# Kernel tuning notes

Hardware: AMD Instinct MI355X
Metric: run time of the kernel (lower is better)

Reference implementation:

```python
import jax, jax.numpy as jnp
import numpy as np

D_MODEL = 2048
NUM_HEADS = 16
HEAD_DIM = D_MODEL // NUM_HEADS
LAYER_IDX = 0
NUM_LAYERS = 13
REINIT_LAMBDA = 0.8


def setup_inputs() -> dict:
    key = jax.random.key(0)
    ks = jax.random.split(key, 8)
    B, S = 2, 2048
    x = jax.random.normal(ks[0], (B, S, D_MODEL), dtype=jnp.float32)
    init = 1.0 / np.sqrt(D_MODEL)
    def w(k):
        return jax.random.uniform(k, (D_MODEL, D_MODEL), dtype=jnp.float32, minval=-init, maxval=init)
    lam_init = REINIT_LAMBDA * ((LAYER_IDX + 1) / NUM_LAYERS)
    return {
        "x": x,
        "q1_w": w(ks[1]), "k1_w": w(ks[2]),
        "q2_w": w(ks[3]), "k2_w": w(ks[4]),
        "v_w": w(ks[5]), "o_w": w(ks[6]),
        "lambda_param": jnp.full((NUM_HEADS,), lam_init, dtype=jnp.float32),
    }


def _heads(t, B, S):
    # [B, S, D] -> [B, H, S, Dh]
    return t.reshape(B, S, NUM_HEADS, HEAD_DIM).transpose(0, 2, 1, 3)


def reference(x, q1_w, k1_w, q2_w, k2_w, v_w, o_w, lambda_param):
    B, S, _ = x.shape
    # nn.Linear(bias=False): y = x @ W.T, W is [out, in]
    q1 = _heads(x @ q1_w.T, B, S)
    k1 = _heads(x @ k1_w.T, B, S)
    q2 = _heads(x @ q2_w.T, B, S)
    k2 = _heads(x @ k2_w.T, B, S)
    v = _heads(x @ v_w.T, B, S)
    scale = jnp.sqrt(jnp.float32(HEAD_DIM))
    attn1 = jax.nn.softmax(jnp.einsum('bhqd,bhkd->bhqk', q1, k1) / scale, axis=-1)
    attn2 = jax.nn.softmax(jnp.einsum('bhqd,bhkd->bhqk', q2, k2) / scale, axis=-1)
    lam = lambda_param.reshape(1, NUM_HEADS, 1, 1)
    out = jnp.einsum('bhqk,bhkd->bhqd', attn1 - lam * attn2, v)
    out = out.transpose(0, 2, 1, 3).reshape(B, S, D_MODEL)
    return out @ o_w.T
```

## Files before the change

### kernel.cpp

```cpp
#include <hip/hip_runtime.h>
#include <hip/hip_bf16.h>
#include <stdint.h>

typedef __bf16 bf16_t;
typedef __bf16 bf16x8 __attribute__((ext_vector_type(8)));
typedef float f32x4 __attribute__((ext_vector_type(4)));

#define D_MODEL 2048
#define SEQ     2048
#define NHEADS  16
#define HDIM    128
#define BATCH   2
#define NTOK    (BATCH * SEQ)
#define NELEM   ((size_t)BATCH * SEQ * D_MODEL)
#define D2      ((size_t)D_MODEL * D_MODEL)

__global__ void __launch_bounds__(256)
cvt7_kernel(const float* __restrict__ x,
            const float* __restrict__ w0, const float* __restrict__ w1,
            const float* __restrict__ w2, const float* __restrict__ w3,
            const float* __restrict__ w4, const float* __restrict__ w5,
            bf16_t* __restrict__ xb, bf16_t* __restrict__ wb) {
  const int y = blockIdx.y;
  const float* srcs[7] = {x, w0, w1, w2, w3, w4, w5};
  const float* src = srcs[y];
  bf16_t* dst = (y == 0) ? xb : wb + (size_t)(y - 1) * D2;
  const size_t n = (y == 0) ? NELEM : D2;
  const size_t base = ((size_t)blockIdx.x * 256 + threadIdx.x) * 8;
  if (base >= n) return;
  f32x4 lo = *(const f32x4*)(src + base);
  f32x4 hi = *(const f32x4*)(src + base + 4);
  union { bf16x8 v; bf16_t h[8]; } u;
#pragma unroll
  for (int j = 0; j < 4; j++) {
    u.h[j]     = (bf16_t)lo[j];
    u.h[j + 4] = (bf16_t)hi[j];
  }
  *(bf16x8*)(dst + base) = u.v;
}

__device__ __forceinline__ void async_load16(const void* g, void* l) {
  __builtin_amdgcn_global_load_lds(
      (const __attribute__((address_space(1))) void*)g,
      (__attribute__((address_space(3))) void*)l, 16, 0, 0);
}

template <int TRANS, typename TC>
__device__ __forceinline__ void gemm_tile_body(const bf16_t* __restrict__ A,
                                               const bf16_t* __restrict__ W,
                                               TC* __restrict__ C) {
  extern __shared__ char smem[];
  bf16_t* As = (bf16_t*)smem;
  bf16_t* Bs = (bf16_t*)smem + 128 * 32;
  const int K = D_MODEL, N = D_MODEL;
  const int tid  = threadIdx.x;
  const int wave = tid >> 6, lane = tid & 63;
  const int quad = lane >> 4, l16 = lane & 15;
  const int tm = blockIdx.x * 128, tn = blockIdx.y * 128;
  const int wm = (wave & 1) * 64, wn = (wave >> 1) * 64;

  f32x4 acc[4][4];
#pragma unroll
  for (int i = 0; i < 4; i++)
#pragma unroll
    for (int j = 0; j < 4; j++) acc[i][j] = (f32x4){0.f, 0.f, 0.f, 0.f};

  const int srow = lane >> 2;
  const int scol = (lane & 3) * 8;

  for (int k0 = 0; k0 < K; k0 += 32) {
    __syncthreads();
#pragma unroll
    for (int i = 0; i < 2; i++) {
      const int rbase = (i * 4 + wave) * 16;
      async_load16(A + (size_t)(tm + rbase + srow) * K + k0 + scol, As + rbase * 32);
      async_load16(W + (size_t)(tn + rbase + srow) * K + k0 + scol, Bs + rbase * 32);
    }
    __syncthreads();

    bf16x8 af[4], bfr[4];
#pragma unroll
    for (int i = 0; i < 4; i++)
      af[i] = *(const bf16x8*)(As + (wm + i * 16 + l16) * 32 + quad * 8);
#pragma unroll
    for (int j = 0; j < 4; j++)
      bfr[j] = *(const bf16x8*)(Bs + (wn + j * 16 + l16) * 32 + quad * 8);
#pragma unroll
    for (int i = 0; i < 4; i++)
#pragma unroll
      for (int j = 0; j < 4; j++)
        acc[i][j] = __builtin_amdgcn_mfma_f32_16x16x32_bf16(af[i], bfr[j], acc[i][j], 0, 0, 0);
  }

#pragma unroll
  for (int i = 0; i < 4; i++) {
    const int r0 = wm + i * 16 + quad * 4;
#pragma unroll
    for (int j = 0; j < 4; j++) {
      const int c = tn + wn + j * 16 + l16;
      if constexpr (TRANS) {
        const int m = tm + r0;
        const int b = m >> 11;
        const int s = m & (SEQ - 1);
        union { bf16_t h[4]; uint2 u2; } p;
#pragma unroll
        for (int r = 0; r < 4; r++) p.h[r] = (bf16_t)acc[i][j][r];
        *(uint2*)((bf16_t*)C + (size_t)(b * D_MODEL + c) * SEQ + s) = p.u2;
      } else {
#pragma unroll
        for (int r = 0; r < 4; r++)
          C[(size_t)(tm + r0 + r) * N + c] = (TC)acc[i][j][r];
      }
    }
  }
}

__global__ void __launch_bounds__(256)
gemm_out_kernel(const bf16_t* __restrict__ A, const bf16_t* __restrict__ W,
                float* __restrict__ C) {
  gemm_tile_body<0, float>(A, W, C);
}

template <int TRANS, typename TC>
__device__ __forceinline__ void gemm256_body(const bf16_t* __restrict__ A,
                                             const bf16_t* __restrict__ W,
                                             TC* __restrict__ C,
                                             const int tm, const int tn) {
  extern __shared__ char smem[];
  constexpr int K = D_MODEL;
  constexpr int NT = K / 64;
  const int tid = threadIdx.x;
  const int wid = tid >> 6, lane = tid & 63;
  const int quad = lane >> 4, l16 = lane & 15;
  const int wm = wid >> 2, wn = wid & 3;

  const int sr = lane >> 2;
  const int sc = (lane & 3) ^ ((lane >> 4) & 2);
  const int rdoff = (l16 * 64 + quad * 16) ^ ((l16 & 8) << 2);

  f32x4 acc[8][4];
#pragma unroll
  for (int i = 0; i < 8; i++)
#pragma unroll
    for (int j = 0; j < 4; j++) acc[i][j] = (f32x4){0.f, 0.f, 0.f, 0.f};

  bf16x8 af[2][4], bfA[2][2], bfB[2][2];

#define STAGE256(P, rowbase, ldsbase, h, t)                                      \
  {                                                                              \
    const bf16_t* _s = (P) + (size_t)((rowbase) + (h) * 128 + wid * 16 + sr) * K \
                           + ((t) * 64 + sc * 8);                                \
    char* _d = smem + (ldsbase) + (h) * 16384 + wid * 2048;                      \
    async_load16(_s, _d);                                                        \
    async_load16(_s + 32, _d + 1024);                                            \
  }

#define LDA256(c, rh)                                                            \
  _Pragma("unroll") for (int ks = 0; ks < 2; ks++)                               \
  _Pragma("unroll") for (int j = 0; j < 4; j++)                                  \
      af[ks][j] = *(const bf16x8*)(smem + (c) * 65536 +                          \
                  ((wm * 8 + (rh) * 4 + j) * 2 + ks) * 1024 + rdoff);

#define LDB256(c, dst, cf0)                                                      \
  _Pragma("unroll") for (int ks = 0; ks < 2; ks++)                               \
  _Pragma("unroll") for (int j = 0; j < 2; j++)                                  \
      dst[ks][j] = *(const bf16x8*)(smem + (c) * 65536 + 32768 +                 \
                   ((wn * 4 + (cf0) + j) * 2 + ks) * 1024 + rdoff);

#define MFMA16(rh, bfr, cb)                                                      \
  _Pragma("unroll") for (int j = 0; j < 4; j++)                                  \
  _Pragma("unroll") for (int cf = 0; cf < 2; cf++)                               \
  _Pragma("unroll") for (int ks = 0; ks < 2; ks++)                               \
      acc[(rh) * 4 + j][(cb) + cf] = __builtin_amdgcn_mfma_f32_16x16x32_bf16(    \
          af[ks][j], bfr[ks][cf], acc[(rh) * 4 + j][(cb) + cf], 0, 0, 0);

#define BAR256() __builtin_amdgcn_s_barrier()
#define LGKM0()                                                                  \
  { asm volatile("s_waitcnt lgkmcnt(0)" ::: "memory");                           \
    __builtin_amdgcn_sched_barrier(0); }
#define VMW4()                                                                   \
  { asm volatile("s_waitcnt vmcnt(4)" ::: "memory");                             \
    __builtin_amdgcn_sched_barrier(0); }
#define VMW0()                                                                   \
  { asm volatile("s_waitcnt vmcnt(0)" ::: "memory");                             \
    __builtin_amdgcn_sched_barrier(0); }

  STAGE256(A, tm, 0,     0, 0); STAGE256(A, tm, 0,     1, 0);
  STAGE256(W, tn, 32768, 0, 0); STAGE256(W, tn, 32768, 1, 0);
  STAGE256(W, tn, 98304, 0, 1); STAGE256(W, tn, 98304, 1, 1);
  VMW4();
  BAR256();

  for (int it = 0; it < NT / 2; ++it) {
    const int kt = 2 * it;
    const int t2 = (kt + 2 < NT) ? kt + 2 : 0;
    const int t3 = (kt + 3 < NT) ? kt + 3 : 0;

    LDA256(0, 0); LDB256(0, bfA, 0);
    STAGE256(A, tm, 65536, 0, kt + 1);
    BAR256(); LGKM0();
    __builtin_amdgcn_s_setprio(1); MFMA16(0, bfA, 0); __builtin_amdgcn_s_setprio(0);
    BAR256();
    LDB256(0, bfB, 2);
    STAGE256(A, tm, 65536, 1, kt + 1);
    BAR256(); LGKM0();
    __builtin_amdgcn_s_setprio(1); MFMA16(0, bfB, 2); __builtin_amdgcn_s_setprio(0);
    BAR256();
    LDA256(0, 1);
    STAGE256(W, tn, 32768, 0, t2);
    BAR256(); LGKM0();
    __builtin_amdgcn_s_setprio(1); MFMA16(1, bfA, 0); __builtin_amdgcn_s_setprio(0);
    BAR256();
    STAGE256(W, tn, 32768, 1, t2);
    BAR256();
    __builtin_amdgcn_s_setprio(1); MFMA16(1, bfB, 2); __builtin_amdgcn_s_setprio(0);
    VMW4();
    BAR256();
    LDA256(1, 0); LDB256(1, bfA, 0);
    STAGE256(A, tm, 0, 0, t2);
    BAR256(); LGKM0();
    __builtin_amdgcn_s_setprio(1); MFMA16(0, bfA, 0); __builtin_amdgcn_s_setprio(0);
    BAR256();
    LDB256(1, bfB, 2);
    STAGE256(A, tm, 0, 1, t2);
    BAR256(); LGKM0();
    __builtin_amdgcn_s_setprio(1); MFMA16(0, bfB, 2); __builtin_amdgcn_s_setprio(0);
    BAR256();
    LDA256(1, 1);
    STAGE256(W, tn, 98304, 0, t3);
    BAR256(); LGKM0();
    __builtin_amdgcn_s_setprio(1); MFMA16(1, bfA, 0); __builtin_amdgcn_s_setprio(0);
    BAR256();
    STAGE256(W, tn, 98304, 1, t3);
    BAR256();
    __builtin_amdgcn_s_setprio(1); MFMA16(1, bfB, 2); __builtin_amdgcn_s_setprio(0);
    VMW4();
    BAR256();
  }
  VMW0();

#pragma unroll
  for (int rf = 0; rf < 8; rf++) {
    const int r0 = wm * 128 + rf * 16 + quad * 4;
#pragma unroll
    for (int cf = 0; cf < 4; cf++) {
      const int c = tn + wn * 64 + cf * 16 + l16;
      if constexpr (TRANS) {
        const int m = tm + r0;
        const int b = m >> 11;
        const int s = m & (SEQ - 1);
        union { bf16_t h[4]; uint2 u2; } p;
#pragma unroll
        for (int r = 0; r < 4; r++) p.h[r] = (bf16_t)acc[rf][cf][r];
        *(uint2*)((bf16_t*)C + (size_t)(b * D_MODEL + c) * SEQ + s) = p.u2;
      } else {
#pragma unroll
        for (int r = 0; r < 4; r++)
          C[(size_t)(tm + r0 + r) * D_MODEL + c] = (TC)acc[rf][cf][r];
      }
    }
  }
#undef STAGE256
#undef LDA256
#undef LDB256
#undef MFMA16
#undef BAR256
#undef LGKM0
#undef VMW4
#undef VMW0
}

__global__ void __launch_bounds__(512, 2)
proj5_kernel(const bf16_t* __restrict__ xb, const bf16_t* __restrict__ wb,
             bf16_t* __restrict__ q1, bf16_t* __restrict__ k1,
             bf16_t* __restrict__ q2, bf16_t* __restrict__ k2,
             bf16_t* __restrict__ vt) {
  const int g = blockIdx.y;
  const int orig = blockIdx.x;
  const int wg = (orig & 7) * 16 + (orig >> 3);
  const int tm = (wg & 15) * 256;
  const int tn = (wg >> 4) * 256;
  const bf16_t* w = wb + (size_t)g * D2;
  if (g == 4) {
    gemm256_body<1, bf16_t>(xb, w, vt, tm, tn);
  } else {
    bf16_t* o = (g == 0) ? q1 : (g == 1) ? k1 : (g == 2) ? q2 : k2;
    gemm256_body<0, bf16_t>(xb, w, o, tm, tn);
  }
}

__global__ void __launch_bounds__(256, 3)
diff_attn_kernel(const bf16_t* __restrict__ q1g, const bf16_t* __restrict__ k1g,
                 const bf16_t* __restrict__ q2g, const bf16_t* __restrict__ k2g,
                 const bf16_t* __restrict__ vtg, const float* __restrict__ lamg,
                 bf16_t* __restrict__ outg) {
  const int blk = blockIdx.x;
  const int xcd = blk & 7;
  const int idx = blk >> 3;
  const int bh  = xcd * 4 + (idx >> 5);
  const int qt  = idx & 31;
  const int b = bh >> 4, h = bh & 15;
  const int tid = threadIdx.x, wave = tid >> 6, lane = tid & 63;
  const int quad = lane >> 4, l16 = lane & 15;
  const int q0 = qt * 64 + wave * 16;

  __shared__ bf16_t K1s[64 * 128];
  __shared__ bf16_t K2s[64 * 128];
  __shared__ bf16_t Vs[128 * 64];

  const bf16_t* q1p = q1g + ((size_t)b * SEQ + q0) * D_MODEL + h * HDIM;
  const bf16_t* q2p = q2g + ((size_t)b * SEQ + q0) * D_MODEL + h * HDIM;
  const bf16_t* k1p = k1g + (size_t)b * SEQ * D_MODEL + h * HDIM;
  const bf16_t* k2p = k2g + (size_t)b * SEQ * D_MODEL + h * HDIM;
  const bf16_t* vtp = vtg + ((size_t)b * D_MODEL + h * HDIM) * SEQ;

  bf16x8 aq1[4], aq2[4];
#pragma unroll
  for (int c = 0; c < 4; c++) {
    aq1[c] = *(const bf16x8*)(q1p + (size_t)l16 * D_MODEL + c * 32 + quad * 8);
    aq2[c] = *(const bf16x8*)(q2p + (size_t)l16 * D_MODEL + c * 32 + quad * 8);
  }

  f32x4 O1[8], O2[8];
#pragma unroll
  for (int n = 0; n < 8; n++) {
    O1[n] = (f32x4){0.f, 0.f, 0.f, 0.f};
    O2[n] = (f32x4){0.f, 0.f, 0.f, 0.f};
  }
  float l1 = 0.f, l2 = 0.f;

  const float c2 = 0.0883883476483184f * 1.4426950408889634f;

  const int k_r  = lane >> 4;
  const int k_p  = lane & 15;
  const int v_r  = lane >> 3;
  const int v_p  = lane & 7;

  for (int kt = 0; kt < SEQ; kt += 64) {
    __syncthreads();
#pragma unroll
    for (int i = 0; i < 4; i++) {
      const int krb = wave * 16 + i * 4;
      const int kr  = krb + k_r;
      const int kkey = (((kr >> 2) & 3) << 3) | (((kr >> 4) & 1) << 2) |
                       (kr & 3) | (kr & 32);
      const int kg = k_p ^ (kr & 7);
      async_load16(k1p + (size_t)(kt + kkey) * D_MODEL + kg * 8, K1s + krb * 128);
      async_load16(k2p + (size_t)(kt + kkey) * D_MODEL + kg * 8, K2s + krb * 128);
      const int vrb = wave * 32 + i * 8;
      const int vr  = vrb + v_r;
      const int vg  = v_p ^ (vr & 7);
      async_load16(vtp + (size_t)vr * SEQ + kt + vg * 8, Vs + vrb * 64);
    }
    __syncthreads();

    f32x4 s1[4], s2[4];
#pragma unroll
    for (int s = 0; s < 4; s++) {
      s1[s] = (f32x4){0.f, 0.f, 0.f, 0.f};
      s2[s] = (f32x4){0.f, 0.f, 0.f, 0.f};
    }
    const int xsw = l16 & 7;
#pragma unroll
    for (int c = 0; c < 4; c++) {
      const int pos = ((c * 4 + quad) ^ xsw) * 8;
#pragma unroll
      for (int s = 0; s < 4; s++) {
        const int rowoff = (s * 16 + l16) * 128;
        bf16x8 f1 = *(const bf16x8*)(K1s + rowoff + pos);
        bf16x8 f2 = *(const bf16x8*)(K2s + rowoff + pos);
        s1[s] = __builtin_amdgcn_mfma_f32_16x16x32_bf16(f1, aq1[c], s1[s], 0, 0, 0);
        s2[s] = __builtin_amdgcn_mfma_f32_16x16x32_bf16(f2, aq2[c], s2[s], 0, 0, 0);
      }
    }

#pragma unroll
    for (int half = 0; half < 2; half++) {
      union { bf16x8 v; bf16_t h[8]; } p1, p2;
#pragma unroll
      for (int r = 0; r < 4; r++) {
        const float e1a = __builtin_amdgcn_exp2f(s1[2 * half][r] * c2);
        const float e1b = __builtin_amdgcn_exp2f(s1[2 * half + 1][r] * c2);
        const float e2a = __builtin_amdgcn_exp2f(s2[2 * half][r] * c2);
        const float e2b = __builtin_amdgcn_exp2f(s2[2 * half + 1][r] * c2);
        p1.h[r] = (bf16_t)e1a; p1.h[4 + r] = (bf16_t)e1b;
        p2.h[r] = (bf16_t)e2a; p2.h[4 + r] = (bf16_t)e2b;
        l1 += e1a + e1b;
        l2 += e2a + e2b;
      }
      const int vpos = ((half * 4 + quad) ^ xsw) * 8;
#pragma unroll
      for (int n = 0; n < 8; n++) {
        bf16x8 vf = *(const bf16x8*)(Vs + (n * 16 + l16) * 64 + vpos);
        O1[n] = __builtin_amdgcn_mfma_f32_16x16x32_bf16(p1.v, vf, O1[n], 0, 0, 0);
        O2[n] = __builtin_amdgcn_mfma_f32_16x16x32_bf16(p2.v, vf, O2[n], 0, 0, 0);
      }
    }
  }

  l1 += __shfl_xor(l1, 16); l1 += __shfl_xor(l1, 32);
  l2 += __shfl_xor(l2, 16); l2 += __shfl_xor(l2, 32);

  const float lam = lamg[h];
  const float i1 = 1.f / l1, i2 = lam / l2;
  float i1o[4], i2o[4];
#pragma unroll
  for (int r = 0; r < 4; r++) {
    i1o[r] = __shfl(i1, quad * 4 + r, 16);
    i2o[r] = __shfl(i2, quad * 4 + r, 16);
  }
  bf16_t* op = outg + ((size_t)b * SEQ + q0) * D_MODEL + h * HDIM;
#pragma unroll
  for (int r = 0; r < 4; r++)
#pragma unroll
    for (int n = 0; n < 8; n++)
      op[(size_t)(quad * 4 + r) * D_MODEL + n * 16 + l16] =
          (bf16_t)(O1[n][r] * i1o[r] - O2[n][r] * i2o[r]);
}

extern "C" void kernel_launch(void* const* d_in, const int* in_sizes, int n_in,
                              void* d_out, int out_size, void* d_ws, size_t ws_size,
                              hipStream_t stream) {
  const float* x   = (const float*)d_in[0];
  const float* wq1 = (const float*)d_in[1];
  const float* wk1 = (const float*)d_in[2];
  const float* wq2 = (const float*)d_in[3];
  const float* wk2 = (const float*)d_in[4];
  const float* wv  = (const float*)d_in[5];
  const float* wo  = (const float*)d_in[6];
  const float* lam = (const float*)d_in[7];

  bf16_t* ws = (bf16_t*)d_ws;
  bf16_t* q1 = ws + 0 * NELEM;
  bf16_t* k1 = ws + 1 * NELEM;
  bf16_t* q2 = ws + 2 * NELEM;
  bf16_t* k2 = ws + 3 * NELEM;
  bf16_t* vt = ws + 4 * NELEM;
  bf16_t* xb = ws + 5 * NELEM;
  bf16_t* ao = xb;
  bf16_t* wb = ws + 6 * NELEM;

  static bool attr_set = false;
  if (!attr_set) {
    (void)hipFuncSetAttribute(reinterpret_cast<const void*>(proj5_kernel),
                              hipFuncAttributeMaxDynamicSharedMemorySize, 131072);
    attr_set = true;
  }

  cvt7_kernel<<<dim3(4096, 7), dim3(256), 0, stream>>>(
      x, wq1, wk1, wq2, wk2, wv, wo, xb, wb);
  proj5_kernel<<<dim3(128, 5), dim3(512), 131072, stream>>>(
      xb, wb, q1, k1, q2, k2, vt);
  diff_attn_kernel<<<dim3(BATCH * NHEADS * (SEQ / 64)), dim3(256), 0, stream>>>(
      q1, k1, q2, k2, vt, lam, ao);
  gemm_out_kernel<<<dim3(NTOK / 128, D_MODEL / 128), dim3(256), 16384, stream>>>(
      ao, wb + 5 * D2, (float*)d_out);
}
```

Baseline: 570.7 us.

## Process 32 query rows per wave in diff attention to reuse K/V fragments

Each wave of the differential attention kernel now handles two 16-row query sets (128 queries per block) rather than one, so every K1/K2/V fragment read from shared memory feeds twice as many MFMAs. The grid is halved and the score computation is restructured per 16-key slice to limit live registers. This cuts LDS traffic and global K/V reloads per query, but doubles the accumulator registers, so occupancy drops to 2 blocks per CU. The smaller grid may also use the CUs less evenly.

```diff
diff --git a/kernel.cpp b/kernel.cpp
--- a/kernel.cpp
+++ b/kernel.cpp
@@ -289,7 +289,7 @@
   }
 }
 
-__global__ void __launch_bounds__(256, 3)
+__global__ void __launch_bounds__(256, 2)
 diff_attn_kernel(const bf16_t* __restrict__ q1g, const bf16_t* __restrict__ k1g,
                  const bf16_t* __restrict__ q2g, const bf16_t* __restrict__ k2g,
                  const bf16_t* __restrict__ vtg, const float* __restrict__ lamg,
@@ -297,12 +297,12 @@
   const int blk = blockIdx.x;
   const int xcd = blk & 7;
   const int idx = blk >> 3;
-  const int bh  = xcd * 4 + (idx >> 5);
-  const int qt  = idx & 31;
+  const int bh  = xcd * 4 + (idx >> 4);
+  const int qt  = idx & 15;
   const int b = bh >> 4, h = bh & 15;
   const int tid = threadIdx.x, wave = tid >> 6, lane = tid & 63;
   const int quad = lane >> 4, l16 = lane & 15;
-  const int q0 = qt * 64 + wave * 16;
+  const int q0 = qt * 128 + wave * 32;
 
   __shared__ bf16_t K1s[64 * 128];
   __shared__ bf16_t K2s[64 * 128];
@@ -314,20 +314,24 @@
   const bf16_t* k2p = k2g + (size_t)b * SEQ * D_MODEL + h * HDIM;
   const bf16_t* vtp = vtg + ((size_t)b * D_MODEL + h * HDIM) * SEQ;
 
-  bf16x8 aq1[4], aq2[4];
-#pragma unroll
-  for (int c = 0; c < 4; c++) {
-    aq1[c] = *(const bf16x8*)(q1p + (size_t)l16 * D_MODEL + c * 32 + quad * 8);
-    aq2[c] = *(const bf16x8*)(q2p + (size_t)l16 * D_MODEL + c * 32 + quad * 8);
-  }
-
-  f32x4 O1[8], O2[8];
-#pragma unroll
-  for (int n = 0; n < 8; n++) {
-    O1[n] = (f32x4){0.f, 0.f, 0.f, 0.f};
-    O2[n] = (f32x4){0.f, 0.f, 0.f, 0.f};
-  }
-  float l1 = 0.f, l2 = 0.f;
+  bf16x8 aq1[2][4], aq2[2][4];
+#pragma unroll
+  for (int set = 0; set < 2; set++)
+#pragma unroll
+    for (int c = 0; c < 4; c++) {
+      aq1[set][c] = *(const bf16x8*)(q1p + (size_t)(set * 16 + l16) * D_MODEL + c * 32 + quad * 8);
+      aq2[set][c] = *(const bf16x8*)(q2p + (size_t)(set * 16 + l16) * D_MODEL + c * 32 + quad * 8);
+    }
+
+  f32x4 O1[2][8], O2[2][8];
+#pragma unroll
+  for (int set = 0; set < 2; set++)
+#pragma unroll
+    for (int n = 0; n < 8; n++) {
+      O1[set][n] = (f32x4){0.f, 0.f, 0.f, 0.f};
+      O2[set][n] = (f32x4){0.f, 0.f, 0.f, 0.f};
+    }
+  float l1[2] = {0.f, 0.f}, l2[2] = {0.f, 0.f};
 
   const float c2 = 0.0883883476483184f * 1.4426950408889634f;
 
@@ -354,68 +358,76 @@
     }
     __syncthreads();
 
-    f32x4 s1[4], s2[4];
-#pragma unroll
-    for (int s = 0; s < 4; s++) {
-      s1[s] = (f32x4){0.f, 0.f, 0.f, 0.f};
-      s2[s] = (f32x4){0.f, 0.f, 0.f, 0.f};
-    }
     const int xsw = l16 & 7;
 #pragma unroll
-    for (int c = 0; c < 4; c++) {
-      const int pos = ((c * 4 + quad) ^ xsw) * 8;
-#pragma unroll
-      for (int s = 0; s < 4; s++) {
+    for (int half = 0; half < 2; half++) {
+      union { bf16x8 v; bf16_t h[8]; } p1[2], p2[2];
+#pragma unroll
+      for (int ss = 0; ss < 2; ss++) {
+        const int s = half * 2 + ss;
         const int rowoff = (s * 16 + l16) * 128;
-        bf16x8 f1 = *(const bf16x8*)(K1s + rowoff + pos);
-        bf16x8 f2 = *(const bf16x8*)(K2s + rowoff + pos);
-        s1[s] = __builtin_amdgcn_mfma_f32_16x16x32_bf16(f1, aq1[c], s1[s], 0, 0, 0);
-        s2[s] = __builtin_amdgcn_mfma_f32_16x16x32_bf16(f2, aq2[c], s2[s], 0, 0, 0);
-      }
-    }
-
-#pragma unroll
-    for (int half = 0; half < 2; half++) {
-      union { bf16x8 v; bf16_t h[8]; } p1, p2;
-#pragma unroll
-      for (int r = 0; r < 4; r++) {
-        const float e1a = __builtin_amdgcn_exp2f(s1[2 * half][r] * c2);
-        const float e1b = __builtin_amdgcn_exp2f(s1[2 * half + 1][r] * c2);
-        const float e2a = __builtin_amdgcn_exp2f(s2[2 * half][r] * c2);
-        const float e2b = __builtin_amdgcn_exp2f(s2[2 * half + 1][r] * c2);
-        p1.h[r] = (bf16_t)e1a; p1.h[4 + r] = (bf16_t)e1b;
-        p2.h[r] = (bf16_t)e2a; p2.h[4 + r] = (bf16_t)e2b;
-        l1 += e1a + e1b;
-        l2 += e2a + e2b;
+        f32x4 sa1 = (f32x4){0.f, 0.f, 0.f, 0.f};
+        f32x4 sb1 = (f32x4){0.f, 0.f, 0.f, 0.f};
+        f32x4 sa2 = (f32x4){0.f, 0.f, 0.f, 0.f};
+        f32x4 sb2 = (f32x4){0.f, 0.f, 0.f, 0.f};
+#pragma unroll
+        for (int c = 0; c < 4; c++) {
+          const int pos = ((c * 4 + quad) ^ xsw) * 8;
+          bf16x8 f1 = *(const bf16x8*)(K1s + rowoff + pos);
+          bf16x8 f2 = *(const bf16x8*)(K2s + rowoff + pos);
+          sa1 = __builtin_amdgcn_mfma_f32_16x16x32_bf16(f1, aq1[0][c], sa1, 0, 0, 0);
+          sb1 = __builtin_amdgcn_mfma_f32_16x16x32_bf16(f1, aq1[1][c], sb1, 0, 0, 0);
+          sa2 = __builtin_amdgcn_mfma_f32_16x16x32_bf16(f2, aq2[0][c], sa2, 0, 0, 0);
+          sb2 = __builtin_amdgcn_mfma_f32_16x16x32_bf16(f2, aq2[1][c], sb2, 0, 0, 0);
+        }
+#pragma unroll
+        for (int r = 0; r < 4; r++) {
+          const float e1a = __builtin_amdgcn_exp2f(sa1[r] * c2);
+          const float e1b = __builtin_amdgcn_exp2f(sb1[r] * c2);
+          const float e2a = __builtin_amdgcn_exp2f(sa2[r] * c2);
+          const float e2b = __builtin_amdgcn_exp2f(sb2[r] * c2);
+          p1[0].h[ss * 4 + r] = (bf16_t)e1a; l1[0] += e1a;
+          p1[1].h[ss * 4 + r] = (bf16_t)e1b; l1[1] += e1b;
+          p2[0].h[ss * 4 + r] = (bf16_t)e2a; l2[0] += e2a;
+          p2[1].h[ss * 4 + r] = (bf16_t)e2b; l2[1] += e2b;
+        }
       }
       const int vpos = ((half * 4 + quad) ^ xsw) * 8;
 #pragma unroll
       for (int n = 0; n < 8; n++) {
         bf16x8 vf = *(const bf16x8*)(Vs + (n * 16 + l16) * 64 + vpos);
-        O1[n] = __builtin_amdgcn_mfma_f32_16x16x32_bf16(p1.v, vf, O1[n], 0, 0, 0);
-        O2[n] = __builtin_amdgcn_mfma_f32_16x16x32_bf16(p2.v, vf, O2[n], 0, 0, 0);
+        O1[0][n] = __builtin_amdgcn_mfma_f32_16x16x32_bf16(p1[0].v, vf, O1[0][n], 0, 0, 0);
+        O1[1][n] = __builtin_amdgcn_mfma_f32_16x16x32_bf16(p1[1].v, vf, O1[1][n], 0, 0, 0);
+        O2[0][n] = __builtin_amdgcn_mfma_f32_16x16x32_bf16(p2[0].v, vf, O2[0][n], 0, 0, 0);
+        O2[1][n] = __builtin_amdgcn_mfma_f32_16x16x32_bf16(p2[1].v, vf, O2[1][n], 0, 0, 0);
       }
     }
   }
 
-  l1 += __shfl_xor(l1, 16); l1 += __shfl_xor(l1, 32);
-  l2 += __shfl_xor(l2, 16); l2 += __shfl_xor(l2, 32);
+#pragma unroll
+  for (int set = 0; set < 2; set++) {
+    l1[set] += __shfl_xor(l1[set], 16); l1[set] += __shfl_xor(l1[set], 32);
+    l2[set] += __shfl_xor(l2[set], 16); l2[set] += __shfl_xor(l2[set], 32);
+  }
 
   const float lam = lamg[h];
-  const float i1 = 1.f / l1, i2 = lam / l2;
-  float i1o[4], i2o[4];
-#pragma unroll
-  for (int r = 0; r < 4; r++) {
-    i1o[r] = __shfl(i1, quad * 4 + r, 16);
-    i2o[r] = __shfl(i2, quad * 4 + r, 16);
-  }
   bf16_t* op = outg + ((size_t)b * SEQ + q0) * D_MODEL + h * HDIM;
 #pragma unroll
-  for (int r = 0; r < 4; r++)
-#pragma unroll
-    for (int n = 0; n < 8; n++)
-      op[(size_t)(quad * 4 + r) * D_MODEL + n * 16 + l16] =
-          (bf16_t)(O1[n][r] * i1o[r] - O2[n][r] * i2o[r]);
+  for (int set = 0; set < 2; set++) {
+    const float i1 = 1.f / l1[set], i2 = lam / l2[set];
+    float i1o[4], i2o[4];
+#pragma unroll
+    for (int r = 0; r < 4; r++) {
+      i1o[r] = __shfl(i1, quad * 4 + r, 16);
+      i2o[r] = __shfl(i2, quad * 4 + r, 16);
+    }
+#pragma unroll
+    for (int r = 0; r < 4; r++)
+#pragma unroll
+      for (int n = 0; n < 8; n++)
+        op[(size_t)(set * 16 + quad * 4 + r) * D_MODEL + n * 16 + l16] =
+            (bf16_t)(O1[set][n][r] * i1o[r] - O2[set][n][r] * i2o[r]);
+  }
 }
 
 extern "C" void kernel_launch(void* const* d_in, const int* in_sizes, int n_in,
@@ -451,7 +463,7 @@
       x, wq1, wk1, wq2, wk2, wv, wo, xb, wb);
   proj5_kernel<<<dim3(128, 5), dim3(512), 131072, stream>>>(
       xb, wb, q1, k1, q2, k2, vt);
-  diff_attn_kernel<<<dim3(BATCH * NHEADS * (SEQ / 64)), dim3(256), 0, stream>>>(
+  diff_attn_kernel<<<dim3(BATCH * NHEADS * (SEQ / 128)), dim3(256), 0, stream>>>(
       q1, k1, q2, k2, vt, lam, ao);
   gemm_out_kernel<<<dim3(NTOK / 128, D_MODEL / 128), dim3(256), 16384, stream>>>(
       ao, wb + 5 * D2, (float*)d_out);
```

Measured after the change: 900.6 us. 1.58x slower.

## Split attention waves by softmax stream, each wave handling 32 query rows

Applied to the files above, without the earlier changes.

Reassigns the four waves in the differential attention kernel so that two waves compute the q1/k1 stream and two compute the q2/k2 stream, each over 32 query rows instead of 16. Each K fragment read from LDS is now reused across two query tiles, which halves K LDS traffic per MFMA. The score computation is interleaved with exp per key sub-tile, which lowers the live score registers. The two streams are combined at the end through an fp32 LDS exchange with an extra barrier, at the cost of an added epilogue sync and LDS round trip.

```diff
diff --git a/kernel.cpp b/kernel.cpp
--- a/kernel.cpp
+++ b/kernel.cpp
@@ -302,32 +302,36 @@
   const int b = bh >> 4, h = bh & 15;
   const int tid = threadIdx.x, wave = tid >> 6, lane = tid & 63;
   const int quad = lane >> 4, l16 = lane & 15;
-  const int q0 = qt * 64 + wave * 16;
-
-  __shared__ bf16_t K1s[64 * 128];
-  __shared__ bf16_t K2s[64 * 128];
-  __shared__ bf16_t Vs[128 * 64];
-
-  const bf16_t* q1p = q1g + ((size_t)b * SEQ + q0) * D_MODEL + h * HDIM;
-  const bf16_t* q2p = q2g + ((size_t)b * SEQ + q0) * D_MODEL + h * HDIM;
+  const int stream = wave >> 1;
+  const int wq     = wave & 1;
+  const int q0 = qt * 64 + wq * 32;
+
+  __shared__ char smem_all[49152];
+  bf16_t* K1s = (bf16_t*)smem_all;
+  bf16_t* K2s = (bf16_t*)(smem_all + 16384);
+  bf16_t* Vs  = (bf16_t*)(smem_all + 32768);
+
   const bf16_t* k1p = k1g + (size_t)b * SEQ * D_MODEL + h * HDIM;
   const bf16_t* k2p = k2g + (size_t)b * SEQ * D_MODEL + h * HDIM;
   const bf16_t* vtp = vtg + ((size_t)b * D_MODEL + h * HDIM) * SEQ;
-
-  bf16x8 aq1[4], aq2[4];
+  const bf16_t* qp  = (stream ? q2g : q1g) +
+                      ((size_t)b * SEQ + q0) * D_MODEL + h * HDIM;
+  const bf16_t* Ksp = stream ? K2s : K1s;
+
+  bf16x8 aqa[4], aqb[4];
 #pragma unroll
   for (int c = 0; c < 4; c++) {
-    aq1[c] = *(const bf16x8*)(q1p + (size_t)l16 * D_MODEL + c * 32 + quad * 8);
-    aq2[c] = *(const bf16x8*)(q2p + (size_t)l16 * D_MODEL + c * 32 + quad * 8);
-  }
-
-  f32x4 O1[8], O2[8];
+    aqa[c] = *(const bf16x8*)(qp + (size_t)l16 * D_MODEL + c * 32 + quad * 8);
+    aqb[c] = *(const bf16x8*)(qp + (size_t)(16 + l16) * D_MODEL + c * 32 + quad * 8);
+  }
+
+  f32x4 Oa[8], Ob[8];
 #pragma unroll
   for (int n = 0; n < 8; n++) {
-    O1[n] = (f32x4){0.f, 0.f, 0.f, 0.f};
-    O2[n] = (f32x4){0.f, 0.f, 0.f, 0.f};
-  }
-  float l1 = 0.f, l2 = 0.f;
+    Oa[n] = (f32x4){0.f, 0.f, 0.f, 0.f};
+    Ob[n] = (f32x4){0.f, 0.f, 0.f, 0.f};
+  }
+  float la = 0.f, lb = 0.f;
 
   const float c2 = 0.0883883476483184f * 1.4426950408889634f;
 
@@ -354,68 +358,86 @@
     }
     __syncthreads();
 
-    f32x4 s1[4], s2[4];
-#pragma unroll
-    for (int s = 0; s < 4; s++) {
-      s1[s] = (f32x4){0.f, 0.f, 0.f, 0.f};
-      s2[s] = (f32x4){0.f, 0.f, 0.f, 0.f};
-    }
     const int xsw = l16 & 7;
 #pragma unroll
-    for (int c = 0; c < 4; c++) {
-      const int pos = ((c * 4 + quad) ^ xsw) * 8;
-#pragma unroll
-      for (int s = 0; s < 4; s++) {
+    for (int half = 0; half < 2; half++) {
+      union { bf16x8 v; bf16_t h[8]; } pa, pb;
+#pragma unroll
+      for (int ss = 0; ss < 2; ss++) {
+        const int s = half * 2 + ss;
         const int rowoff = (s * 16 + l16) * 128;
-        bf16x8 f1 = *(const bf16x8*)(K1s + rowoff + pos);
-        bf16x8 f2 = *(const bf16x8*)(K2s + rowoff + pos);
-        s1[s] = __builtin_amdgcn_mfma_f32_16x16x32_bf16(f1, aq1[c], s1[s], 0, 0, 0);
-        s2[s] = __builtin_amdgcn_mfma_f32_16x16x32_bf16(f2, aq2[c], s2[s], 0, 0, 0);
-      }
-    }
-
-#pragma unroll
-    for (int half = 0; half < 2; half++) {
-      union { bf16x8 v; bf16_t h[8]; } p1, p2;
-#pragma unroll
-      for (int r = 0; r < 4; r++) {
-        const float e1a = __builtin_amdgcn_exp2f(s1[2 * half][r] * c2);
-        const float e1b = __builtin_amdgcn_exp2f(s1[2 * half + 1][r] * c2);
-        const float e2a = __builtin_amdgcn_exp2f(s2[2 * half][r] * c2);
-        const float e2b = __builtin_amdgcn_exp2f(s2[2 * half + 1][r] * c2);
-        p1.h[r] = (bf16_t)e1a; p1.h[4 + r] = (bf16_t)e1b;
-        p2.h[r] = (bf16_t)e2a; p2.h[4 + r] = (bf16_t)e2b;
-        l1 += e1a + e1b;
-        l2 += e2a + e2b;
+        f32x4 sa = (f32x4){0.f, 0.f, 0.f, 0.f};
+        f32x4 sb = (f32x4){0.f, 0.f, 0.f, 0.f};
+#pragma unroll
+        for (int c = 0; c < 4; c++) {
+          const int pos = ((c * 4 + quad) ^ xsw) * 8;
+          bf16x8 f = *(const bf16x8*)(Ksp + rowoff + pos);
+          sa = __builtin_amdgcn_mfma_f32_16x16x32_bf16(f, aqa[c], sa, 0, 0, 0);
+          sb = __builtin_amdgcn_mfma_f32_16x16x32_bf16(f, aqb[c], sb, 0, 0, 0);
+        }
+#pragma unroll
+        for (int r = 0; r < 4; r++) {
+          const float ea = __builtin_amdgcn_exp2f(sa[r] * c2);
+          const float eb = __builtin_amdgcn_exp2f(sb[r] * c2);
+          pa.h[ss * 4 + r] = (bf16_t)ea; la += ea;
+          pb.h[ss * 4 + r] = (bf16_t)eb; lb += eb;
+        }
       }
       const int vpos = ((half * 4 + quad) ^ xsw) * 8;
 #pragma unroll
       for (int n = 0; n < 8; n++) {
         bf16x8 vf = *(const bf16x8*)(Vs + (n * 16 + l16) * 64 + vpos);
-        O1[n] = __builtin_amdgcn_mfma_f32_16x16x32_bf16(p1.v, vf, O1[n], 0, 0, 0);
-        O2[n] = __builtin_amdgcn_mfma_f32_16x16x32_bf16(p2.v, vf, O2[n], 0, 0, 0);
-      }
-    }
-  }
-
-  l1 += __shfl_xor(l1, 16); l1 += __shfl_xor(l1, 32);
-  l2 += __shfl_xor(l2, 16); l2 += __shfl_xor(l2, 32);
-
-  const float lam = lamg[h];
-  const float i1 = 1.f / l1, i2 = lam / l2;
-  float i1o[4], i2o[4];
-#pragma unroll
-  for (int r = 0; r < 4; r++) {
-    i1o[r] = __shfl(i1, quad * 4 + r, 16);
-    i2o[r] = __shfl(i2, quad * 4 + r, 16);
-  }
-  bf16_t* op = outg + ((size_t)b * SEQ + q0) * D_MODEL + h * HDIM;
-#pragma unroll
-  for (int r = 0; r < 4; r++)
-#pragma unroll
-    for (int n = 0; n < 8; n++)
-      op[(size_t)(quad * 4 + r) * D_MODEL + n * 16 + l16] =
-          (bf16_t)(O1[n][r] * i1o[r] - O2[n][r] * i2o[r]);
+        Oa[n] = __builtin_amdgcn_mfma_f32_16x16x32_bf16(pa.v, vf, Oa[n], 0, 0, 0);
+        Ob[n] = __builtin_amdgcn_mfma_f32_16x16x32_bf16(pb.v, vf, Ob[n], 0, 0, 0);
+      }
+    }
+  }
+
+  la += __shfl_xor(la, 16); la += __shfl_xor(la, 32);
+  lb += __shfl_xor(lb, 16); lb += __shfl_xor(lb, 32);
+
+  __syncthreads();
+  float* xfer = (float*)smem_all;
+
+  if (stream == 1) {
+    const float lam = lamg[h];
+    const float ia = lam / la, ib = lam / lb;
+    float iao[4], ibo[4];
+#pragma unroll
+    for (int r = 0; r < 4; r++) {
+      iao[r] = __shfl(ia, quad * 4 + r, 16);
+      ibo[r] = __shfl(ib, quad * 4 + r, 16);
+    }
+#pragma unroll
+    for (int r = 0; r < 4; r++)
+#pragma unroll
+      for (int n = 0; n < 8; n++) {
+        xfer[(wq * 32 + quad * 4 + r) * 128 + n * 16 + l16] = Oa[n][r] * iao[r];
+        xfer[(wq * 32 + 16 + quad * 4 + r) * 128 + n * 16 + l16] = Ob[n][r] * ibo[r];
+      }
+  }
+  __syncthreads();
+  if (stream == 0) {
+    const float ia = 1.f / la, ib = 1.f / lb;
+    float iao[4], ibo[4];
+#pragma unroll
+    for (int r = 0; r < 4; r++) {
+      iao[r] = __shfl(ia, quad * 4 + r, 16);
+      ibo[r] = __shfl(ib, quad * 4 + r, 16);
+    }
+    bf16_t* op = outg + ((size_t)b * SEQ + q0) * D_MODEL + h * HDIM;
+#pragma unroll
+    for (int r = 0; r < 4; r++)
+#pragma unroll
+      for (int n = 0; n < 8; n++) {
+        const float va = Oa[n][r] * iao[r] -
+                         xfer[(wq * 32 + quad * 4 + r) * 128 + n * 16 + l16];
+        const float vb = Ob[n][r] * ibo[r] -
+                         xfer[(wq * 32 + 16 + quad * 4 + r) * 128 + n * 16 + l16];
+        op[(size_t)(quad * 4 + r) * D_MODEL + n * 16 + l16] = (bf16_t)va;
+        op[(size_t)(16 + quad * 4 + r) * D_MODEL + n * 16 + l16] = (bf16_t)vb;
+      }
+  }
 }
 
 extern "C" void kernel_launch(void* const* d_in, const int* in_sizes, int n_in,
```

Result: slower. 627.2 us (+9.9%).
